# Performance work log

Hardware: AMD Instinct MI355X
Metric: run time of the kernel (lower is better)

Reference implementation:

```python
import jax, jax.numpy as jnp
import numpy as np

VOCAB = 50257
EMBED = 256
NFREQ = 64
NRULES = 100
B, S = 4, 1024


def setup_inputs() -> dict:
    key = jax.random.key(0)
    ks = jax.random.split(key, 7)
    return {
        "token_ids": jax.random.randint(ks[0], (B, S), 0, VOCAB),
        "a_n": jax.random.normal(ks[1], (VOCAB, NFREQ), dtype=jnp.float32),
        "b_n": jax.random.normal(ks[2], (VOCAB, NFREQ), dtype=jnp.float32),
        "rule_transform": jax.random.normal(ks[3], (NRULES, EMBED, EMBED), dtype=jnp.float32),
        "token_rules": jax.random.randint(ks[4], (VOCAB,), 0, NRULES),
        "proj_w": jax.random.normal(ks[5], (EMBED, NFREQ), dtype=jnp.float32) * (1.0 / np.sqrt(NFREQ)),
        "proj_b": jax.random.normal(ks[6], (EMBED,), dtype=jnp.float32) * 0.01,
    }


def reference(token_ids, a_n, b_n, rule_transform, token_rules, proj_w, proj_b):
    vocab_size, nfreq = a_n.shape
    # fourier_freqs = linspace(1, F, F) -> [1..F]
    freqs = jnp.arange(1, nfreq + 1, dtype=jnp.float32)  # [F]
    x = token_ids.astype(jnp.float32)[..., None] / vocab_size  # [B,S,1]
    ang = (2.0 * jnp.pi) * freqs * x  # [B,S,F]
    # gather per-token fourier coefficients, fuse cos/sin combine
    fourier = a_n[token_ids] * jnp.cos(ang) + b_n[token_ids] * jnp.sin(ang)  # [B,S,F]
    base = jnp.einsum('bsf,df->bsd', fourier, proj_w) + proj_b  # [B,S,D]
    rule_idx = token_rules[token_ids]  # [B,S]
    rules = rule_transform[rule_idx]  # [B,S,D,D] gathered per token
    return jnp.einsum('bsd,bsde->bse', base, rules)  # [B,S,D]
```

## Files before the change

### kernel.cpp

```cpp
#include <hip/hip_runtime.h>
#include <math.h>

#define VOCAB   50257
#define EMBED   256
#define NFREQ   64
#define NRULES  100
#define NTOK    4096
#define CAP     256
#define CHUNK   16
#define NCHUNK  (CAP / CHUNK)

#define BASE_BYTES ((size_t)NTOK * EMBED * 4)

__global__ void zero_counts_kernel(int* __restrict__ counts) {
    if (threadIdx.x < NRULES) counts[threadIdx.x] = 0;
}

__global__ __launch_bounds__(256) void fourier_kernel(
    const int*   __restrict__ token_ids,
    const float* __restrict__ a_n,
    const float* __restrict__ b_n,
    const int*   __restrict__ token_rules,
    float*       __restrict__ fourier,
    int*         __restrict__ counts,
    int*         __restrict__ list)
{
    const int t   = blockIdx.x * 4 + (threadIdx.x >> 6);
    const int f   = threadIdx.x & 63;
    const int tok = token_ids[t];

    const float x = (float)tok / (float)VOCAB;
    float sv, cv;
    sincosf(6.283185307179586f * (float)(f + 1) * x, &sv, &cv);
    fourier[t * NFREQ + f] = a_n[tok * NFREQ + f] * cv
                           + b_n[tok * NFREQ + f] * sv;

    if (f == 0) {
        const int rule = token_rules[tok];
        const int pos  = atomicAdd(&counts[rule], 1);
        if (pos < CAP) list[rule * CAP + pos] = t;
    }
}

__global__ __launch_bounds__(256) void base_kernel(
    const float* __restrict__ fourier,
    const float* __restrict__ proj_w,
    const float* __restrict__ proj_b,
    float*       __restrict__ base)
{
    __shared__ float s_wT[NFREQ * EMBED];
    const int tid = threadIdx.x;

    const float4* __restrict__ W4 = (const float4*)proj_w;
    #pragma unroll
    for (int i = 0; i < 16; ++i) {
        const int v = i * 256 + tid;
        const float4 w = W4[v];
        const int d  = v >> 4;
        const int f0 = (v & 15) * 4;
        s_wT[(f0 + 0) * EMBED + (d ^ ((f0 + 0) & 31))] = w.x;
        s_wT[(f0 + 1) * EMBED + (d ^ ((f0 + 1) & 31))] = w.y;
        s_wT[(f0 + 2) * EMBED + (d ^ ((f0 + 2) & 31))] = w.z;
        s_wT[(f0 + 3) * EMBED + (d ^ ((f0 + 3) & 31))] = w.w;
    }
    __syncthreads();

    const int tok0 = blockIdx.x * 16;
    const int d    = tid;
    const float bias = proj_b[d];
    float acc[16];
    #pragma unroll
    for (int t = 0; t < 16; ++t) acc[t] = bias;

    #pragma unroll 4
    for (int fq = 0; fq < 16; ++fq) {
        float wv[4];
        #pragma unroll
        for (int j = 0; j < 4; ++j) {
            const int f = fq * 4 + j;
            wv[j] = s_wT[f * EMBED + (d ^ (f & 31))];
        }
        #pragma unroll
        for (int t = 0; t < 16; ++t) {
            const float4 fv =
                ((const float4*)(fourier + (size_t)(tok0 + t) * NFREQ))[fq];
            acc[t] += wv[0] * fv.x + wv[1] * fv.y + wv[2] * fv.z + wv[3] * fv.w;
        }
    }
    #pragma unroll
    for (int t = 0; t < 16; ++t)
        base[(size_t)(tok0 + t) * EMBED + d] = acc[t];
}

__global__ __launch_bounds__(256) void apply_kernel(
    const float* __restrict__ base,
    const float* __restrict__ rule_transform,
    const int*   __restrict__ counts,
    const int*   __restrict__ list,
    float*       __restrict__ out)
{
    __shared__ float s_red[3 * CHUNK * 4 * 64];

    const int rule = blockIdx.x;
    int cnt = counts[rule];
    if (cnt > CAP) cnt = CAP;
    const int t0 = blockIdx.y * CHUNK;
    if (t0 >= cnt) return;

    const int w  = threadIdx.x >> 6;
    const int eq = threadIdx.x & 63;

    int idx[CHUNK];
    #pragma unroll
    for (int t = 0; t < CHUNK; ++t) {
        int tt = t0 + t;
        if (tt > cnt - 1) tt = cnt - 1;
        idx[t] = __builtin_amdgcn_readfirstlane(list[rule * CAP + tt]);
    }

    const float4* __restrict__ T4 =
        (const float4*)(rule_transform + (size_t)rule * EMBED * EMBED);

    float acc[CHUNK][4];
    #pragma unroll
    for (int t = 0; t < CHUNK; ++t) {
        acc[t][0] = 0.f; acc[t][1] = 0.f; acc[t][2] = 0.f; acc[t][3] = 0.f;
    }

    const int d0 = w * 64;
    for (int dq = 0; dq < 16; ++dq) {
        float4 bv[CHUNK];
        #pragma unroll
        for (int t = 0; t < CHUNK; ++t)
            bv[t] = *(const float4*)(base + (size_t)idx[t] * EMBED + d0 + dq * 4);
        #pragma unroll
        for (int i = 0; i < 4; ++i) {
            const float4 tv = T4[(size_t)(d0 + dq * 4 + i) * 64 + eq];
            #pragma unroll
            for (int t = 0; t < CHUNK; ++t) {
                const float b = (i == 0) ? bv[t].x : (i == 1) ? bv[t].y
                              : (i == 2) ? bv[t].z : bv[t].w;
                acc[t][0] += b * tv.x;
                acc[t][1] += b * tv.y;
                acc[t][2] += b * tv.z;
                acc[t][3] += b * tv.w;
            }
        }
    }

    if (w > 0) {
        #pragma unroll
        for (int t = 0; t < CHUNK; ++t)
            #pragma unroll
            for (int c = 0; c < 4; ++c)
                s_red[(((w - 1) * CHUNK + t) * 4 + c) * 64 + eq] = acc[t][c];
    }
    __syncthreads();
    if (w == 0) {
        #pragma unroll
        for (int t = 0; t < CHUNK; ++t) {
            if (t0 + t < cnt) {
                float r[4];
                #pragma unroll
                for (int c = 0; c < 4; ++c) {
                    r[c] = acc[t][c]
                         + s_red[((0 * CHUNK + t) * 4 + c) * 64 + eq]
                         + s_red[((1 * CHUNK + t) * 4 + c) * 64 + eq]
                         + s_red[((2 * CHUNK + t) * 4 + c) * 64 + eq];
                }
                ((float4*)(out + (size_t)idx[t] * EMBED))[eq] =
                    make_float4(r[0], r[1], r[2], r[3]);
            }
        }
    }
}

extern "C" void kernel_launch(void* const* d_in, const int* in_sizes, int n_in,
                              void* d_out, int out_size, void* d_ws, size_t ws_size,
                              hipStream_t stream) {
    const int*   token_ids      = (const int*)  d_in[0];
    const float* a_n            = (const float*)d_in[1];
    const float* b_n            = (const float*)d_in[2];
    const float* rule_transform = (const float*)d_in[3];
    const int*   token_rules    = (const int*)  d_in[4];
    const float* proj_w         = (const float*)d_in[5];
    const float* proj_b         = (const float*)d_in[6];
    float*       out            = (float*)d_out;

    float* base    = (float*)d_ws;
    int*   counts  = (int*)((char*)d_ws + BASE_BYTES);
    int*   list    = (int*)((char*)d_ws + BASE_BYTES + 512);
    float* fourier = out;

    zero_counts_kernel<<<1, 128, 0, stream>>>(counts);
    fourier_kernel<<<NTOK / 4, 256, 0, stream>>>(
        token_ids, a_n, b_n, token_rules, fourier, counts, list);
    base_kernel<<<NTOK / 16, 256, 0, stream>>>(fourier, proj_w, proj_b, base);
    apply_kernel<<<dim3(NRULES, NCHUNK), 256, 0, stream>>>(
        base, rule_transform, counts, list, out);
}
```

Measured before the change: 149.6 us.

## Fuse fourier into base kernel and stage gathered base rows in LDS

Merges the fourier computation into the projection kernel, so per-token Fourier features go to shared memory instead of a global round trip, and replaces the zeroing kernel with hipMemsetAsync. The apply kernel now stages the 16 gathered base rows in LDS once and software-prefetches the next rule_transform rows into registers. This removes one launch and redundant global gathers, at the cost of an extra barrier and more register pressure from the prefetch buffers.

```diff
diff --git a/kernel.cpp b/kernel.cpp
--- a/kernel.cpp
+++ b/kernel.cpp
@@ -12,43 +12,20 @@
 
 #define BASE_BYTES ((size_t)NTOK * EMBED * 4)
 
-__global__ void zero_counts_kernel(int* __restrict__ counts) {
-    if (threadIdx.x < NRULES) counts[threadIdx.x] = 0;
-}
-
-__global__ __launch_bounds__(256) void fourier_kernel(
+__global__ __launch_bounds__(256) void fused_base_kernel(
     const int*   __restrict__ token_ids,
     const float* __restrict__ a_n,
     const float* __restrict__ b_n,
     const int*   __restrict__ token_rules,
-    float*       __restrict__ fourier,
+    const float* __restrict__ proj_w,
+    const float* __restrict__ proj_b,
+    float*       __restrict__ base,
     int*         __restrict__ counts,
     int*         __restrict__ list)
 {
-    const int t   = blockIdx.x * 4 + (threadIdx.x >> 6);
-    const int f   = threadIdx.x & 63;
-    const int tok = token_ids[t];
-
-    const float x = (float)tok / (float)VOCAB;
-    float sv, cv;
-    sincosf(6.283185307179586f * (float)(f + 1) * x, &sv, &cv);
-    fourier[t * NFREQ + f] = a_n[tok * NFREQ + f] * cv
-                           + b_n[tok * NFREQ + f] * sv;
-
-    if (f == 0) {
-        const int rule = token_rules[tok];
-        const int pos  = atomicAdd(&counts[rule], 1);
-        if (pos < CAP) list[rule * CAP + pos] = t;
-    }
-}
-
-__global__ __launch_bounds__(256) void base_kernel(
-    const float* __restrict__ fourier,
-    const float* __restrict__ proj_w,
-    const float* __restrict__ proj_b,
-    float*       __restrict__ base)
-{
     __shared__ float s_wT[NFREQ * EMBED];
+    __shared__ float s_four[16][NFREQ];
+
     const int tid = threadIdx.x;
 
     const float4* __restrict__ W4 = (const float4*)proj_w;
@@ -63,33 +40,54 @@
         s_wT[(f0 + 2) * EMBED + (d ^ ((f0 + 2) & 31))] = w.z;
         s_wT[(f0 + 3) * EMBED + (d ^ ((f0 + 3) & 31))] = w.w;
     }
-    __syncthreads();
-
-    const int tok0 = blockIdx.x * 16;
-    const int d    = tid;
+
+    const int t_local = tid >> 4;
+    const int fq      = tid & 15;
+    const int tok_idx = blockIdx.x * 16 + t_local;
+    const int tok     = token_ids[tok_idx];
+
+    const float4 a4 = ((const float4*)(a_n + (size_t)tok * NFREQ))[fq];
+    const float4 b4 = ((const float4*)(b_n + (size_t)tok * NFREQ))[fq];
+    const float  x  = (float)tok / (float)VOCAB;
+    const float  w0 = 6.283185307179586f * x;
+
+    float4 fv; float sv, cv;
+    sincosf(w0 * (float)(fq * 4 + 1), &sv, &cv); fv.x = a4.x * cv + b4.x * sv;
+    sincosf(w0 * (float)(fq * 4 + 2), &sv, &cv); fv.y = a4.y * cv + b4.y * sv;
+    sincosf(w0 * (float)(fq * 4 + 3), &sv, &cv); fv.z = a4.z * cv + b4.z * sv;
+    sincosf(w0 * (float)(fq * 4 + 4), &sv, &cv); fv.w = a4.w * cv + b4.w * sv;
+    ((float4*)s_four[t_local])[fq] = fv;
+
+    if (fq == 0) {
+        const int rule = token_rules[tok];
+        const int pos  = atomicAdd(&counts[rule], 1);
+        if (pos < CAP) list[rule * CAP + pos] = tok_idx;
+    }
+    __syncthreads();
+
+    const int   d    = tid;
     const float bias = proj_b[d];
     float acc[16];
     #pragma unroll
     for (int t = 0; t < 16; ++t) acc[t] = bias;
 
     #pragma unroll 4
-    for (int fq = 0; fq < 16; ++fq) {
+    for (int q = 0; q < 16; ++q) {
         float wv[4];
         #pragma unroll
         for (int j = 0; j < 4; ++j) {
-            const int f = fq * 4 + j;
+            const int f = q * 4 + j;
             wv[j] = s_wT[f * EMBED + (d ^ (f & 31))];
         }
         #pragma unroll
         for (int t = 0; t < 16; ++t) {
-            const float4 fv =
-                ((const float4*)(fourier + (size_t)(tok0 + t) * NFREQ))[fq];
-            acc[t] += wv[0] * fv.x + wv[1] * fv.y + wv[2] * fv.z + wv[3] * fv.w;
+            const float4 f4 = ((const float4*)s_four[t])[q];
+            acc[t] += wv[0] * f4.x + wv[1] * f4.y + wv[2] * f4.z + wv[3] * f4.w;
         }
     }
     #pragma unroll
     for (int t = 0; t < 16; ++t)
-        base[(size_t)(tok0 + t) * EMBED + d] = acc[t];
+        base[(size_t)(blockIdx.x * 16 + t) * EMBED + d] = acc[t];
 }
 
 __global__ __launch_bounds__(256) void apply_kernel(
@@ -99,7 +97,8 @@
     const int*   __restrict__ list,
     float*       __restrict__ out)
 {
-    __shared__ float s_red[3 * CHUNK * 4 * 64];
+    __shared__ float s_mem[3 * CHUNK * 4 * 64];
+    float* s_base = s_mem;
 
     const int rule = blockIdx.x;
     int cnt = counts[rule];
@@ -118,6 +117,11 @@
         idx[t] = __builtin_amdgcn_readfirstlane(list[rule * CAP + tt]);
     }
 
+    #pragma unroll
+    for (int t = 0; t < CHUNK; ++t)
+        s_base[t * EMBED + threadIdx.x] = base[(size_t)idx[t] * EMBED + threadIdx.x];
+    __syncthreads();
+
     const float4* __restrict__ T4 =
         (const float4*)(rule_transform + (size_t)rule * EMBED * EMBED);
 
@@ -128,48 +132,56 @@
     }
 
     const int d0 = w * 64;
+    float4 tv[4], tvn[4];
+    #pragma unroll
+    for (int i = 0; i < 4; ++i)
+        tv[i] = T4[(size_t)(d0 + i) * 64 + eq];
+
     for (int dq = 0; dq < 16; ++dq) {
-        float4 bv[CHUNK];
-        #pragma unroll
-        for (int t = 0; t < CHUNK; ++t)
-            bv[t] = *(const float4*)(base + (size_t)idx[t] * EMBED + d0 + dq * 4);
-        #pragma unroll
-        for (int i = 0; i < 4; ++i) {
-            const float4 tv = T4[(size_t)(d0 + dq * 4 + i) * 64 + eq];
+        if (dq < 15) {
             #pragma unroll
-            for (int t = 0; t < CHUNK; ++t) {
-                const float b = (i == 0) ? bv[t].x : (i == 1) ? bv[t].y
-                              : (i == 2) ? bv[t].z : bv[t].w;
-                acc[t][0] += b * tv.x;
-                acc[t][1] += b * tv.y;
-                acc[t][2] += b * tv.z;
-                acc[t][3] += b * tv.w;
-            }
-        }
-    }
-
+            for (int i = 0; i < 4; ++i)
+                tvn[i] = T4[(size_t)(d0 + (dq + 1) * 4 + i) * 64 + eq];
+        }
+        #pragma unroll
+        for (int t = 0; t < CHUNK; ++t) {
+            const float4 b4 = *(const float4*)&s_base[t * EMBED + d0 + dq * 4];
+            acc[t][0] += b4.x * tv[0].x + b4.y * tv[1].x + b4.z * tv[2].x + b4.w * tv[3].x;
+            acc[t][1] += b4.x * tv[0].y + b4.y * tv[1].y + b4.z * tv[2].y + b4.w * tv[3].y;
+            acc[t][2] += b4.x * tv[0].z + b4.y * tv[1].z + b4.z * tv[2].z + b4.w * tv[3].z;
+            acc[t][3] += b4.x * tv[0].w + b4.y * tv[1].w + b4.z * tv[2].w + b4.w * tv[3].w;
+        }
+        #pragma unroll
+        for (int i = 0; i < 4; ++i) tv[i] = tvn[i];
+    }
+
+    __syncthreads();
     if (w > 0) {
         #pragma unroll
         for (int t = 0; t < CHUNK; ++t)
             #pragma unroll
             for (int c = 0; c < 4; ++c)
-                s_red[(((w - 1) * CHUNK + t) * 4 + c) * 64 + eq] = acc[t][c];
+                s_mem[(((w - 1) * CHUNK + t) * 4 + c) * 64 + eq] = acc[t][c];
     }
     __syncthreads();
     if (w == 0) {
         #pragma unroll
         for (int t = 0; t < CHUNK; ++t) {
             if (t0 + t < cnt) {
-                float r[4];
-                #pragma unroll
-                for (int c = 0; c < 4; ++c) {
-                    r[c] = acc[t][c]
-                         + s_red[((0 * CHUNK + t) * 4 + c) * 64 + eq]
-                         + s_red[((1 * CHUNK + t) * 4 + c) * 64 + eq]
-                         + s_red[((2 * CHUNK + t) * 4 + c) * 64 + eq];
-                }
+                float r0 = acc[t][0] + s_mem[((0 * CHUNK + t) * 4 + 0) * 64 + eq]
+                                     + s_mem[((1 * CHUNK + t) * 4 + 0) * 64 + eq]
+                                     + s_mem[((2 * CHUNK + t) * 4 + 0) * 64 + eq];
+                float r1 = acc[t][1] + s_mem[((0 * CHUNK + t) * 4 + 1) * 64 + eq]
+                                     + s_mem[((1 * CHUNK + t) * 4 + 1) * 64 + eq]
+                                     + s_mem[((2 * CHUNK + t) * 4 + 1) * 64 + eq];
+                float r2 = acc[t][2] + s_mem[((0 * CHUNK + t) * 4 + 2) * 64 + eq]
+                                     + s_mem[((1 * CHUNK + t) * 4 + 2) * 64 + eq]
+                                     + s_mem[((2 * CHUNK + t) * 4 + 2) * 64 + eq];
+                float r3 = acc[t][3] + s_mem[((0 * CHUNK + t) * 4 + 3) * 64 + eq]
+                                     + s_mem[((1 * CHUNK + t) * 4 + 3) * 64 + eq]
+                                     + s_mem[((2 * CHUNK + t) * 4 + 3) * 64 + eq];
                 ((float4*)(out + (size_t)idx[t] * EMBED))[eq] =
-                    make_float4(r[0], r[1], r[2], r[3]);
+                    make_float4(r0, r1, r2, r3);
             }
         }
     }
@@ -187,15 +199,13 @@
     const float* proj_b         = (const float*)d_in[6];
     float*       out            = (float*)d_out;
 
-    float* base    = (float*)d_ws;
-    int*   counts  = (int*)((char*)d_ws + BASE_BYTES);
-    int*   list    = (int*)((char*)d_ws + BASE_BYTES + 512);
-    float* fourier = out;
-
-    zero_counts_kernel<<<1, 128, 0, stream>>>(counts);
-    fourier_kernel<<<NTOK / 4, 256, 0, stream>>>(
-        token_ids, a_n, b_n, token_rules, fourier, counts, list);
-    base_kernel<<<NTOK / 16, 256, 0, stream>>>(fourier, proj_w, proj_b, base);
+    float* base   = (float*)d_ws;
+    int*   counts = (int*)((char*)d_ws + BASE_BYTES);
+    int*   list   = (int*)((char*)d_ws + BASE_BYTES + 512);
+
+    hipMemsetAsync(counts, 0, NRULES * sizeof(int), stream);
+    fused_base_kernel<<<NTOK / 16, 256, 0, stream>>>(
+        token_ids, a_n, b_n, token_rules, proj_w, proj_b, base, counts, list);
     apply_kernel<<<dim3(NRULES, NCHUNK), 256, 0, stream>>>(
         base, rule_transform, counts, list, out);
 }
```

After: 136.4 us. -8.8%, faster.
